# Performance work log

Hardware: AMD Instinct MI355X
Metric: run time of the kernel (lower is better)

Reference implementation:

```python
import jax, jax.numpy as jnp
import numpy as np

NUM_ENVS = 16384
NUM_AGENTS = 16
IN_DIM = 128
GCN_H = 64
RNN_H = 64
E_PER_GRAPH = 128
N_FEAT = 4   # num_individual_actions_features
N_CAT = 8    # num_action_categories
OUT_DIM = NUM_AGENTS * N_FEAT * N_CAT


def setup_inputs() -> dict:
    key = jax.random.key(0)
    ks = jax.random.split(key, 10)
    x = jax.random.normal(ks[0], (NUM_ENVS, NUM_AGENTS, IN_DIM), dtype=jnp.float32)
    edge_index = jax.random.randint(ks[1], (NUM_ENVS, 2, E_PER_GRAPH), 0, NUM_AGENTS, dtype=jnp.int64)
    prev_h = jax.random.normal(ks[2], (NUM_ENVS, NUM_AGENTS, RNN_H), dtype=jnp.float32)
    s = 0.05
    W_gcn = jax.random.normal(ks[3], (IN_DIM, GCN_H), dtype=jnp.float32) * s
    b_gcn = jnp.zeros((GCN_H,), dtype=jnp.float32)
    W_ih = jax.random.normal(ks[4], (3 * RNN_H, GCN_H), dtype=jnp.float32) * s
    W_hh = jax.random.normal(ks[5], (3 * RNN_H, RNN_H), dtype=jnp.float32) * s
    b_ih = jax.random.normal(ks[6], (3 * RNN_H,), dtype=jnp.float32) * s
    b_hh = jax.random.normal(ks[7], (3 * RNN_H,), dtype=jnp.float32) * s
    W_lin = jax.random.normal(ks[8], (OUT_DIM, NUM_AGENTS * RNN_H), dtype=jnp.float32) * s
    b_lin = jax.random.normal(ks[9], (OUT_DIM,), dtype=jnp.float32) * s
    return {"x": x, "edge_index": edge_index, "prev_rnn_hidden_state": prev_h,
            "W_gcn": W_gcn, "b_gcn": b_gcn, "W_ih": W_ih, "W_hh": W_hh,
            "b_ih": b_ih, "b_hh": b_hh, "W_lin": W_lin, "b_lin": b_lin}


def _forward(x, edge_index, prev_h, W_gcn, b_gcn, W_ih, W_hh, b_ih, b_hh, W_lin, b_lin):
    num_envs = x.shape[0]
    N = num_envs * NUM_AGENTS  # flattened node count
    x_flat = x.reshape(N, IN_DIM)

    # block-offset trick: one big disconnected graph
    offsets = (jnp.arange(num_envs, dtype=edge_index.dtype) * NUM_AGENTS)[:, None, None]  # [env,1,1]
    ei = (edge_index + offsets).reshape(num_envs, 2, -1)  # offsets broadcast over [env,2,E]
    row = ei[:, 0, :].reshape(-1)  # source nodes, [env*E]
    col = ei[:, 1, :].reshape(-1)  # target nodes

    # GCNConv: xw = x @ W; add self-loops; sym-normalize; scatter-add to targets
    xw = x_flat @ W_gcn  # [N, GCN_H]
    ones_e = jnp.ones(row.shape[0], dtype=x.dtype)
    deg = jnp.ones((N,), dtype=x.dtype) + jax.ops.segment_sum(ones_e, col, num_segments=N)
    dinv = jax.lax.rsqrt(deg)
    norm = dinv[row] * dinv[col]  # [env*E]
    msg = norm[:, None] * xw[row]  # gather + scale
    agg = jnp.zeros_like(xw).at[col].add(msg)
    agg = agg + xw / deg[:, None]  # self-loop term: 1/deg * xw
    gcn_out = agg + b_gcn  # [N, GCN_H]

    # single-step GRU (torch gate order: r, z, n)
    h = prev_h.reshape(N, RNN_H)
    gx = gcn_out @ W_ih.T + b_ih  # [N, 3H]
    gh = h @ W_hh.T + b_hh
    rx, zx, nx = jnp.split(gx, 3, axis=-1)
    rh, zh, nh = jnp.split(gh, 3, axis=-1)
    r = jax.nn.sigmoid(rx + rh)
    z = jax.nn.sigmoid(zx + zh)
    n = jnp.tanh(nx + r * nh)
    h_new = (1.0 - z) * n + z * h  # [N, H]

    flat = h_new.reshape(num_envs, NUM_AGENTS * RNN_H)
    logits = flat @ W_lin.T + b_lin  # [env, OUT_DIM]
    next_h = h_new.reshape(num_envs, NUM_AGENTS, RNN_H)
    return logits, next_h


def reference(x, edge_index, prev_rnn_hidden_state, W_gcn, b_gcn, W_ih, W_hh, b_ih, b_hh, W_lin, b_lin):
    return _forward(x, edge_index, prev_rnn_hidden_state, W_gcn, b_gcn, W_ih, W_hh, b_ih, b_hh, W_lin, b_lin)
```

## Files before the change

### kernel.cpp

```cpp
#include <hip/hip_runtime.h>
#include <math.h>

namespace {

constexpr int NUM_ENVS = 16384;
constexpr int OUT_DIM = 512;
constexpr int FLAT = 1024;

typedef float floatx4 __attribute__((ext_vector_type(4)));
typedef short shortx8 __attribute__((ext_vector_type(8)));

#define WAVE_FENCE() asm volatile("s_waitcnt lgkmcnt(0)" ::: "memory")

__device__ __forceinline__ float fast_sigmoid(float v) {
    const float e = __builtin_amdgcn_exp2f(-v * 1.44269504088896340736f);
    return __builtin_amdgcn_rcpf(1.0f + e);
}
__device__ __forceinline__ float fast_tanh(float v) {
    const float e = __builtin_amdgcn_exp2f(v * 2.88539008177792681472f);
    return 1.0f - 2.0f * __builtin_amdgcn_rcpf(1.0f + e);
}
__device__ __forceinline__ unsigned short f2bf(float f) {
    unsigned int u = __float_as_uint(f);
    u = (u + 0x7FFFu + ((u >> 16) & 1u)) >> 16;
    return (unsigned short)u;
}
__device__ __forceinline__ float bf2f(unsigned short s) {
    return __uint_as_float(((unsigned int)s) << 16);
}
__device__ __forceinline__ shortx8 pack8(const float4& f0, const float4& f1) {
    shortx8 o;
    o[0] = (short)f2bf(f0.x); o[1] = (short)f2bf(f0.y);
    o[2] = (short)f2bf(f0.z); o[3] = (short)f2bf(f0.w);
    o[4] = (short)f2bf(f1.x); o[5] = (short)f2bf(f1.y);
    o[6] = (short)f2bf(f1.z); o[7] = (short)f2bf(f1.w);
    return o;
}

constexpr int WS_FLAG = 0;
constexpr int WS_WGF  = 64;
constexpr int WS_WCF  = WS_WGF + 4096;
constexpr int WS_WLB  = WS_WCF + 12288;
constexpr int WS_GB   = WS_WLB + 262144;

__global__ void prep_kernel(const int* __restrict__ edges_i32,
                            const float* __restrict__ Wg,
                            const float* __restrict__ Wih,
                            const float* __restrict__ Whh,
                            const float* __restrict__ Wlin,
                            float* __restrict__ ws) {
    if (blockIdx.x == 0) {
        __shared__ int any_nonzero;
        if (threadIdx.x == 0) any_nonzero = 0;
        __syncthreads();
        if (threadIdx.x < 128 && edges_i32[2 * threadIdx.x + 1] != 0)
            atomicOr(&any_nonzero, 1);
        __syncthreads();
        if (threadIdx.x == 0) ((int*)ws)[WS_FLAG] = (any_nonzero == 0) ? 1 : 0;
        return;
    }
    const int t = ((int)blockIdx.x - 1) * 256 + (int)threadIdx.x;
    if (t < 8192) {
        const int jj = t & 7, lane = (t >> 3) & 63, slot = t >> 9;
        const int nt = slot >> 2, ks = slot & 3;
        const int n = nt * 16 + (lane & 15);
        const int k = ks * 32 + ((lane >> 4) & 3) * 8 + jj;
        ((unsigned short*)(ws + WS_WGF))[t] = f2bf(Wg[k * 64 + n]);
    } else if (t < 32768) {
        const int u = t - 8192;
        const int jj = u & 7, lane = (u >> 3) & 63, slot = u >> 9;
        const int q8 = ((lane >> 4) & 3) * 8 + jj;
        float val;
        if (slot < 16) {
            const int nt = slot >> 2, ks = slot & 3;
            const int n = nt * 16 + (lane & 15);
            const int k = ks * 32 + q8;
            val = (k < 64) ? Wih[n * 64 + k] : Whh[n * 64 + (k - 64)];
        } else if (slot < 32) {
            const int s = slot - 16, nt = s >> 2, ks = s & 3;
            const int n = 64 + nt * 16 + (lane & 15);
            const int k = ks * 32 + q8;
            val = (k < 64) ? Wih[n * 64 + k] : Whh[n * 64 + (k - 64)];
        } else if (slot < 40) {
            const int s = slot - 32, nt = s >> 1, ks = s & 1;
            const int n = 128 + nt * 16 + (lane & 15);
            val = Wih[n * 64 + ks * 32 + q8];
        } else {
            const int s = slot - 40, nt = s >> 1, ks = s & 1;
            const int n = 128 + nt * 16 + (lane & 15);
            val = Whh[n * 64 + ks * 32 + q8];
        }
        ((unsigned short*)(ws + WS_WCF))[u] = f2bf(val);
    } else if (t < 32768 + 524288) {
        const int u = t - 32768;
        ((unsigned short*)(ws + WS_WLB))[u] = f2bf(Wlin[u]);
    }
}

__global__ __launch_bounds__(256, 4) void fused_gcn_gru_kernel(
    const float* __restrict__ x,
    const void*  __restrict__ edges,
    const unsigned short* __restrict__ WgF,
    const float* __restrict__ bg,
    const float* __restrict__ h_prev,
    const unsigned short* __restrict__ WcF,
    const float* __restrict__ bih,
    const float* __restrict__ bhh,
    float* __restrict__ next_h,
    unsigned short* __restrict__ hb,
    const int* __restrict__ flag64)
{
    const int b = blockIdx.x;
    const int tid = threadIdx.x;
    const int lane = tid & 63;
    const int w = tid >> 6;
    const int env = b * 4 + w;

    __shared__ float xw_s[4][16 * 68];
    __shared__ unsigned short A_s[4][16 * 136];
    __shared__ float adj_s[4][16][17];
    __shared__ int   deg_s[4][16];
    __shared__ float dinv_s[4][16];
    __shared__ float invdeg_s[4][16];

    const int ar = lane & 15;
    const int aq = lane >> 4;

    float4 xf[4][2];
    #pragma unroll
    for (int ks = 0; ks < 4; ++ks) {
        const float4* p = (const float4*)(x + ((size_t)env * 16 + ar) * 128 + ks * 32 + aq * 8);
        xf[ks][0] = p[0];
        xf[ks][1] = p[1];
    }
    float4 hf[4];
    {
        const float4* src = (const float4*)(h_prev + ((size_t)env * 16 + ar) * 64 + aq * 16);
        hf[0] = src[0]; hf[1] = src[1]; hf[2] = src[2]; hf[3] = src[3];
    }
    const bool is64 = (*flag64 != 0);
    int rv[2], cv[2];
    const size_t ebase = (size_t)env * 256;
    #pragma unroll
    for (int t = 0; t < 2; ++t) {
        const int idx = lane + 64 * t;
        long long rvl, cvl;
        if (is64) {
            rvl = ((const long long*)edges)[ebase + idx];
            cvl = ((const long long*)edges)[ebase + 128 + idx];
        } else {
            rvl = ((const int*)edges)[ebase + idx];
            cvl = ((const int*)edges)[ebase + 128 + idx];
        }
        rv[t] = (int)rvl & 15;
        cv[t] = (int)cvl & 15;
    }

    {
        float* ap = &adj_s[w][0][0];
        #pragma unroll
        for (int i = 0; i < 5; ++i) {
            const int j = lane + 64 * i;
            if (j < 272) ap[j] = 0.0f;
        }
        if (lane < 16) deg_s[w][lane] = 0;
    }
    {
        unsigned short* dp = &A_s[w][ar * 136 + 64 + aq * 16];
        *(shortx8*)dp = pack8(hf[0], hf[1]);
        *(shortx8*)(dp + 8) = pack8(hf[2], hf[3]);
    }
    WAVE_FENCE();

    #pragma unroll
    for (int t = 0; t < 2; ++t) atomicAdd(&deg_s[w][cv[t]], 1);

    shortx8 afr[4];
    #pragma unroll
    for (int ks = 0; ks < 4; ++ks) afr[ks] = pack8(xf[ks][0], xf[ks][1]);
    floatx4 acc[4];
    #pragma unroll
    for (int nt = 0; nt < 4; ++nt) acc[nt] = (floatx4)(0.0f);
    #pragma unroll
    for (int nt = 0; nt < 4; ++nt) {
        #pragma unroll
        for (int ks = 0; ks < 4; ++ks) {
            const shortx8 bfr = *(const shortx8*)&WgF[((nt * 4 + ks) * 64 + lane) * 8];
            acc[nt] = __builtin_amdgcn_mfma_f32_16x16x32_bf16(afr[ks], bfr, acc[nt], 0, 0, 0);
        }
    }
    WAVE_FENCE();

    if (lane < 16) {
        const float d = 1.0f + (float)deg_s[w][lane];
        dinv_s[w][lane] = rsqrtf(d);
        invdeg_s[w][lane] = 1.0f / d;
    }
    #pragma unroll
    for (int nt = 0; nt < 4; ++nt)
        #pragma unroll
        for (int i = 0; i < 4; ++i)
            xw_s[w][(aq * 4 + i) * 68 + nt * 16 + ar] = acc[nt][i];
    WAVE_FENCE();

    #pragma unroll
    for (int t = 0; t < 2; ++t)
        atomicAdd(&adj_s[w][cv[t]][rv[t]], dinv_s[w][rv[t]] * dinv_s[w][cv[t]]);
    if (lane < 16)
        atomicAdd(&adj_s[w][lane][lane], invdeg_s[w][lane]);
    WAVE_FENCE();

    {
        const int cl = lane >> 2, q = lane & 3;
        float accs[16];
        #pragma unroll
        for (int m = 0; m < 16; ++m) accs[m] = 0.0f;
        for (int r16 = 0; r16 < 16; ++r16) {
            const float a = adj_s[w][cl][r16];
            const float4* xr = (const float4*)&xw_s[w][r16 * 68 + q * 16];
            #pragma unroll
            for (int jq = 0; jq < 4; ++jq) {
                const float4 v = xr[jq];
                accs[4 * jq + 0] += a * v.x;
                accs[4 * jq + 1] += a * v.y;
                accs[4 * jq + 2] += a * v.z;
                accs[4 * jq + 3] += a * v.w;
            }
        }
        unsigned short* dst = &A_s[w][cl * 136 + q * 16];
        shortx8 o0, o1;
        #pragma unroll
        for (int m = 0; m < 8; ++m) o0[m] = (short)f2bf(accs[m] + bg[q * 16 + m]);
        #pragma unroll
        for (int m = 0; m < 8; ++m) o1[m] = (short)f2bf(accs[8 + m] + bg[q * 16 + 8 + m]);
        *(shortx8*)dst = o0;
        *(shortx8*)(dst + 8) = o1;
    }
    WAVE_FENCE();

    shortx8 gfr[4];
    gfr[0] = *(const shortx8*)&A_s[w][ar * 136 + aq * 8];
    gfr[1] = *(const shortx8*)&A_s[w][ar * 136 + 32 + aq * 8];
    gfr[2] = *(const shortx8*)&A_s[w][ar * 136 + 64 + aq * 8];
    gfr[3] = *(const shortx8*)&A_s[w][ar * 136 + 96 + aq * 8];
    floatx4 aR[4], aZ[4], aNX[4], aNH[4];
    #pragma unroll
    for (int nt = 0; nt < 4; ++nt) {
        aR[nt] = (floatx4)(0.0f); aZ[nt] = (floatx4)(0.0f);
        aNX[nt] = (floatx4)(0.0f); aNH[nt] = (floatx4)(0.0f);
    }
    #pragma unroll
    for (int nt = 0; nt < 4; ++nt) {
        #pragma unroll
        for (int ks = 0; ks < 4; ++ks) {
            const shortx8 bfr = *(const shortx8*)&WcF[((nt * 4 + ks) * 64 + lane) * 8];
            aR[nt] = __builtin_amdgcn_mfma_f32_16x16x32_bf16(gfr[ks], bfr, aR[nt], 0, 0, 0);
        }
        #pragma unroll
        for (int ks = 0; ks < 4; ++ks) {
            const shortx8 bfr = *(const shortx8*)&WcF[((16 + nt * 4 + ks) * 64 + lane) * 8];
            aZ[nt] = __builtin_amdgcn_mfma_f32_16x16x32_bf16(gfr[ks], bfr, aZ[nt], 0, 0, 0);
        }
        #pragma unroll
        for (int ks = 0; ks < 2; ++ks) {
            const shortx8 bfr = *(const shortx8*)&WcF[((32 + nt * 2 + ks) * 64 + lane) * 8];
            aNX[nt] = __builtin_amdgcn_mfma_f32_16x16x32_bf16(gfr[ks], bfr, aNX[nt], 0, 0, 0);
        }
        #pragma unroll
        for (int ks = 0; ks < 2; ++ks) {
            const shortx8 bfr = *(const shortx8*)&WcF[((40 + nt * 2 + ks) * 64 + lane) * 8];
            aNH[nt] = __builtin_amdgcn_mfma_f32_16x16x32_bf16(gfr[ks + 2], bfr, aNH[nt], 0, 0, 0);
        }
    }

    const int cl2 = lane & 15;
    const int rq = lane >> 4;
    #pragma unroll
    for (int tp = 0; tp < 4; ++tp) {
        const int f = tp * 16 + cl2;
        const float br = bih[f] + bhh[f];
        const float bz = bih[64 + f] + bhh[64 + f];
        const float bnx = bih[128 + f];
        const float bnh = bhh[128 + f];
        #pragma unroll
        for (int i = 0; i < 4; ++i) {
            const int rl = rq * 4 + i;
            const size_t row = (size_t)env * 16 + rl;
            const float hp = bf2f(A_s[w][rl * 136 + 64 + f]);
            const float r = fast_sigmoid(aR[tp][i] + br);
            const float z = fast_sigmoid(aZ[tp][i] + bz);
            const float n = fast_tanh(aNX[tp][i] + bnx + r * (aNH[tp][i] + bnh));
            const float hv = (1.0f - z) * n + z * hp;
            next_h[row * 64 + f] = hv;
            hb[row * 64 + f] = f2bf(hv);
        }
    }
}

__global__ __launch_bounds__(256, 2) void logits_mfma_kernel(
    const unsigned short* __restrict__ A,
    const unsigned short* __restrict__ B,
    const float* __restrict__ bias,
    float* __restrict__ C)
{
    __shared__ __align__(16) unsigned short As[2][128 * 64];
    __shared__ __align__(16) unsigned short Bs[2][128 * 64];

    const int tid = threadIdx.x;
    const int lane = tid & 63;
    const int wave = tid >> 6;
    const int wr = wave >> 1;
    const int wc = wave & 1;
    const int m0 = blockIdx.y * 128;
    const int n0 = blockIdx.x * 128;
    const int lr = tid >> 3;
    const int lk = tid & 7;

    floatx4 acc[4][4];
    #pragma unroll
    for (int i = 0; i < 4; ++i)
        #pragma unroll
        for (int jn = 0; jn < 4; ++jn)
            acc[i][jn] = (floatx4)(0.0f);

    uint4 ra[4], rb[4];
    auto load_tile = [&](int kt) {
        const int k0 = kt * 64;
        #pragma unroll
        for (int i = 0; i < 4; ++i) {
            const int r = lr + 32 * i;
            ra[i] = *(const uint4*)&A[(size_t)(m0 + r) * FLAT + k0 + lk * 8];
            rb[i] = *(const uint4*)&B[(size_t)(n0 + r) * FLAT + k0 + lk * 8];
        }
    };
    auto write_tile = [&](int buf) {
        #pragma unroll
        for (int i = 0; i < 4; ++i) {
            const int r = lr + 32 * i;
            *(uint4*)&As[buf][r * 64 + ((lk ^ (r & 7)) * 8)] = ra[i];
            *(uint4*)&Bs[buf][r * 64 + ((lk ^ (r & 7)) * 8)] = rb[i];
        }
    };

    load_tile(0);
    write_tile(0);
    __syncthreads();

    #pragma unroll 2
    for (int kt = 0; kt < 16; ++kt) {
        const int cur = kt & 1;
        if (kt < 15) load_tile(kt + 1);
        #pragma unroll
        for (int s = 0; s < 2; ++s) {
            const int kg = s * 4 + (lane >> 4);
            const int sw = (kg ^ (lane & 7)) * 8;
            shortx8 af[4], bf[4];
            #pragma unroll
            for (int t = 0; t < 4; ++t) {
                af[t] = *(const shortx8*)&As[cur][(wr * 64 + t * 16 + (lane & 15)) * 64 + sw];
                bf[t] = *(const shortx8*)&Bs[cur][(wc * 64 + t * 16 + (lane & 15)) * 64 + sw];
            }
            #pragma unroll
            for (int mt = 0; mt < 4; ++mt)
                #pragma unroll
                for (int nt = 0; nt < 4; ++nt)
                    acc[mt][nt] = __builtin_amdgcn_mfma_f32_16x16x32_bf16(
                        af[mt], bf[nt], acc[mt][nt], 0, 0, 0);
        }
        if (kt < 15) {
            write_tile(cur ^ 1);
            __syncthreads();
        }
    }

    const int col_l = lane & 15;
    const int rg = lane >> 4;
    #pragma unroll
    for (int nt = 0; nt < 4; ++nt) {
        const int col = n0 + wc * 64 + nt * 16 + col_l;
        const float bv = bias[col];
        #pragma unroll
        for (int mt = 0; mt < 4; ++mt) {
            const int row = m0 + wr * 64 + mt * 16 + rg * 4;
            #pragma unroll
            for (int i = 0; i < 4; ++i) {
                C[(size_t)(row + i) * OUT_DIM + col] = acc[mt][nt][i] + bv;
            }
        }
    }
}

}

extern "C" void kernel_launch(void* const* d_in, const int* in_sizes, int n_in,
                              void* d_out, int out_size, void* d_ws, size_t ws_size,
                              hipStream_t stream) {
    const float* x    = (const float*)d_in[0];
    const void*  ei   = d_in[1];
    const float* h0   = (const float*)d_in[2];
    const float* Wg   = (const float*)d_in[3];
    const float* bg   = (const float*)d_in[4];
    const float* Wih  = (const float*)d_in[5];
    const float* Whh  = (const float*)d_in[6];
    const float* bih  = (const float*)d_in[7];
    const float* bhh  = (const float*)d_in[8];
    const float* Wlin = (const float*)d_in[9];
    const float* blin = (const float*)d_in[10];

    float* out = (float*)d_out;
    float* logits = out;
    float* next_h = out + (size_t)NUM_ENVS * OUT_DIM;

    float* wsf = (float*)d_ws;
    int* flag = (int*)(wsf + WS_FLAG);
    unsigned short* WgF = (unsigned short*)(wsf + WS_WGF);
    unsigned short* WcF = (unsigned short*)(wsf + WS_WCF);
    unsigned short* Wlb = (unsigned short*)(wsf + WS_WLB);
    unsigned short* gb  = (unsigned short*)(wsf + WS_GB);

    prep_kernel<<<2177, 256, 0, stream>>>((const int*)ei, Wg, Wih, Whh, Wlin, wsf);
    fused_gcn_gru_kernel<<<4096, 256, 0, stream>>>(x, ei, WgF, bg, h0, WcF, bih, bhh,
                                                   next_h, gb, flag);
    dim3 g2(OUT_DIM / 128, NUM_ENVS / 128);
    logits_mfma_kernel<<<g2, 256, 0, stream>>>(gb, Wlb, blin, logits);
}
```

Before: 395.1 us.

## Compute GCN aggregation with split-bf16 MFMA directly from registers

Replaces the scalar FMA loop that multiplied the 16x16 normalized adjacency by the xw tile staged in LDS with three 16x16x16 bf16 MFMAs per column tile. A hi/lo bf16 split of both operands keeps precision close to fp32. This drops the xw_s and invdeg_s LDS buffers, which lowers LDS use and lets launch bounds rise from 4 to 6 blocks per SM. The cost is extra conversion work, and the tighter register budget risks spills.

Result: slower. 433.0 us (+9.6%).

```diff
diff --git a/kernel.cpp b/kernel.cpp
--- a/kernel.cpp
+++ b/kernel.cpp
@@ -9,6 +9,7 @@
 
 typedef float floatx4 __attribute__((ext_vector_type(4)));
 typedef short shortx8 __attribute__((ext_vector_type(8)));
+typedef short shortx4 __attribute__((ext_vector_type(4)));
 
 #define WAVE_FENCE() asm volatile("s_waitcnt lgkmcnt(0)" ::: "memory")
 
@@ -97,7 +98,7 @@
     }
 }
 
-__global__ __launch_bounds__(256, 4) void fused_gcn_gru_kernel(
+__global__ __launch_bounds__(256, 6) void fused_gcn_gru_kernel(
     const float* __restrict__ x,
     const void*  __restrict__ edges,
     const unsigned short* __restrict__ WgF,
@@ -116,12 +117,10 @@
     const int w = tid >> 6;
     const int env = b * 4 + w;
 
-    __shared__ float xw_s[4][16 * 68];
     __shared__ unsigned short A_s[4][16 * 136];
-    __shared__ float adj_s[4][16][17];
+    __shared__ float adj_s[4][16][20];
     __shared__ int   deg_s[4][16];
     __shared__ float dinv_s[4][16];
-    __shared__ float invdeg_s[4][16];
 
     const int ar = lane & 15;
     const int aq = lane >> 4;
@@ -159,13 +158,8 @@
     {
         float* ap = &adj_s[w][0][0];
         #pragma unroll
-        for (int i = 0; i < 5; ++i) {
-            const int j = lane + 64 * i;
-            if (j < 272) ap[j] = 0.0f;
-        }
+        for (int i = 0; i < 5; ++i) ap[lane + 64 * i] = 0.0f;
         if (lane < 16) deg_s[w][lane] = 0;
-    }
-    {
         unsigned short* dp = &A_s[w][ar * 136 + 64 + aq * 16];
         *(shortx8*)dp = pack8(hf[0], hf[1]);
         *(shortx8*)(dp + 8) = pack8(hf[2], hf[3]);
@@ -191,51 +185,53 @@
     }
     WAVE_FENCE();
 
+    float my_invdeg = 0.0f;
     if (lane < 16) {
         const float d = 1.0f + (float)deg_s[w][lane];
         dinv_s[w][lane] = rsqrtf(d);
-        invdeg_s[w][lane] = 1.0f / d;
-    }
-    #pragma unroll
-    for (int nt = 0; nt < 4; ++nt)
-        #pragma unroll
-        for (int i = 0; i < 4; ++i)
-            xw_s[w][(aq * 4 + i) * 68 + nt * 16 + ar] = acc[nt][i];
+        my_invdeg = 1.0f / d;
+    }
     WAVE_FENCE();
 
     #pragma unroll
     for (int t = 0; t < 2; ++t)
         atomicAdd(&adj_s[w][cv[t]][rv[t]], dinv_s[w][rv[t]] * dinv_s[w][cv[t]]);
     if (lane < 16)
-        atomicAdd(&adj_s[w][lane][lane], invdeg_s[w][lane]);
+        atomicAdd(&adj_s[w][lane][lane], my_invdeg);
     WAVE_FENCE();
 
+    shortx4 adjh, adjl;
     {
-        const int cl = lane >> 2, q = lane & 3;
-        float accs[16];
-        #pragma unroll
-        for (int m = 0; m < 16; ++m) accs[m] = 0.0f;
-        for (int r16 = 0; r16 < 16; ++r16) {
-            const float a = adj_s[w][cl][r16];
-            const float4* xr = (const float4*)&xw_s[w][r16 * 68 + q * 16];
-            #pragma unroll
-            for (int jq = 0; jq < 4; ++jq) {
-                const float4 v = xr[jq];
-                accs[4 * jq + 0] += a * v.x;
-                accs[4 * jq + 1] += a * v.y;
-                accs[4 * jq + 2] += a * v.z;
-                accs[4 * jq + 3] += a * v.w;
-            }
-        }
-        unsigned short* dst = &A_s[w][cl * 136 + q * 16];
-        shortx8 o0, o1;
-        #pragma unroll
-        for (int m = 0; m < 8; ++m) o0[m] = (short)f2bf(accs[m] + bg[q * 16 + m]);
-        #pragma unroll
-        for (int m = 0; m < 8; ++m) o1[m] = (short)f2bf(accs[8 + m] + bg[q * 16 + 8 + m]);
-        *(shortx8*)dst = o0;
-        *(shortx8*)(dst + 8) = o1;
-    }
+        const float4 av = *(const float4*)&adj_s[w][ar][aq * 4];
+        #pragma unroll
+        for (int j = 0; j < 4; ++j) {
+            const float v = (&av.x)[j];
+            const unsigned short h = f2bf(v);
+            adjh[j] = (short)h;
+            adjl[j] = (short)f2bf(v - bf2f(h));
+        }
+    }
+    floatx4 agg[4];
+    #pragma unroll
+    for (int nt = 0; nt < 4; ++nt) {
+        shortx4 bh, bl;
+        #pragma unroll
+        for (int j = 0; j < 4; ++j) {
+            const float v = acc[nt][j];
+            const unsigned short h = f2bf(v);
+            bh[j] = (short)h;
+            bl[j] = (short)f2bf(v - bf2f(h));
+        }
+        agg[nt] = (floatx4)(bg[nt * 16 + ar]);
+        agg[nt] = __builtin_amdgcn_mfma_f32_16x16x16bf16_1k(adjh, bh, agg[nt], 0, 0, 0);
+        agg[nt] = __builtin_amdgcn_mfma_f32_16x16x16bf16_1k(adjh, bl, agg[nt], 0, 0, 0);
+        agg[nt] = __builtin_amdgcn_mfma_f32_16x16x16bf16_1k(adjl, bh, agg[nt], 0, 0, 0);
+    }
+    #pragma unroll
+    for (int nt = 0; nt < 4; ++nt)
+        #pragma unroll
+        for (int i = 0; i < 4; ++i)
+            A_s[w][(aq * 4 + i) * 136 + nt * 16 + ar] = f2bf(agg[nt][i]);
     WAVE_FENCE();
 
     shortx8 gfr[4];
```
